# Optimization experiments

Hardware: AMD Instinct MI355X
Metric: run time of the kernel (lower is better)

## Reference

```python
import jax, jax.numpy as jnp
import numpy as np

N = 20000   # genes
E = 160000  # directed edges (self-loops added in forward, as PyG GATv2Conv does by default)
D = 64      # input feature dim
H1, C1 = 8, 128  # conv1 heads / channels
LRELU_SLOPE = 0.2
LN_EPS = 1e-5


def setup_inputs() -> dict:
    key = jax.random.key(0)
    ks = jax.random.split(key, 20)
    s = 0.05
    inp = {
        "x": jax.random.normal(ks[0], (N, D), dtype=jnp.float32),
        "edge_index": jax.random.randint(ks[1], (2, E), 0, N, dtype=jnp.int64),
        # conv1 (GATv2Conv D -> H1*C1, concat)
        "Wl1": jax.random.normal(ks[2], (D, H1 * C1), dtype=jnp.float32) * s,
        "bl1": jax.random.normal(ks[3], (H1 * C1,), dtype=jnp.float32) * s,
        "Wr1": jax.random.normal(ks[4], (D, H1 * C1), dtype=jnp.float32) * s,
        "br1": jax.random.normal(ks[5], (H1 * C1,), dtype=jnp.float32) * s,
        "att1": jax.random.normal(ks[6], (H1, C1), dtype=jnp.float32) * s,
        "b1": jax.random.normal(ks[7], (H1 * C1,), dtype=jnp.float32) * s,
        # skip Linear(D -> H1*C1)
        "Wskip": jax.random.normal(ks[8], (D, H1 * C1), dtype=jnp.float32) * s,
        "bskip": jax.random.normal(ks[9], (H1 * C1,), dtype=jnp.float32) * s,
        # LayerNorm(H1*C1)
        "g1": jnp.ones((H1 * C1,), dtype=jnp.float32),
        "beta1": jnp.zeros((H1 * C1,), dtype=jnp.float32),
        # conv2 (GATv2Conv H1*C1 -> 2, heads=1, concat=False)
        "Wl2": jax.random.normal(ks[10], (H1 * C1, 2), dtype=jnp.float32) * s,
        "bl2": jax.random.normal(ks[11], (2,), dtype=jnp.float32) * s,
        "Wr2": jax.random.normal(ks[12], (H1 * C1, 2), dtype=jnp.float32) * s,
        "br2": jax.random.normal(ks[13], (2,), dtype=jnp.float32) * s,
        "att2": jax.random.normal(ks[14], (1, 2), dtype=jnp.float32) * s,
        "b2": jax.random.normal(ks[15], (2,), dtype=jnp.float32) * s,
    }
    return inp


def _gatv2(x, src, dst, Wl, bl, Wr, br, att, bias, heads, ch, concat):
    """PyG GATv2Conv (eval mode): message src -> dst, scatter-softmax over dst."""
    n = x.shape[0]
    xl = (x @ Wl + bl).reshape(n, heads, ch)  # source-side transform
    xr = (x @ Wr + br).reshape(n, heads, ch)  # target-side transform
    e = jax.nn.leaky_relu(xl[src] + xr[dst], LRELU_SLOPE)   # [E,H,C]
    alpha = jnp.einsum('ehc,hc->eh', e, att)                 # [E,H]
    amax = jax.ops.segment_max(alpha, dst, num_segments=n)   # [N,H]
    ex = jnp.exp(alpha - amax[dst])
    denom = jax.ops.segment_sum(ex, dst, num_segments=n)
    alpha = ex / (denom[dst] + 1e-16)
    msg = xl[src] * alpha[..., None]                          # [E,H,C]
    out = jax.ops.segment_sum(msg, dst, num_segments=n)      # [N,H,C]
    out = out.reshape(n, heads * ch) if concat else out.mean(axis=1)
    return out + bias


def _layernorm(x, g, b):
    mu = x.mean(axis=-1, keepdims=True)
    var = ((x - mu) ** 2).mean(axis=-1, keepdims=True)
    return (x - mu) * jax.lax.rsqrt(var + LN_EPS) * g + b


def reference(x, edge_index, Wl1, bl1, Wr1, br1, att1, b1, Wskip, bskip,
              g1, beta1, Wl2, bl2, Wr2, br2, att2, b2):
    n = x.shape[0]
    loop = jnp.arange(n, dtype=edge_index.dtype)  # add_self_loops=True (PyG default)
    src = jnp.concatenate([edge_index[0], loop])
    dst = jnp.concatenate([edge_index[1], loop])
    x1 = _gatv2(x, src, dst, Wl1, bl1, Wr1, br1, att1, b1, H1, C1, True) + (x @ Wskip + bskip)
    x1 = jax.nn.elu(_layernorm(x1, g1, beta1))
    # dropout is a no-op in eval mode
    return _gatv2(x1, src, dst, Wl2, bl2, Wr2, br2, att2, b2, 1, 2, False)
```

## Files before the change

### kernel.cpp

```cpp
#include <hip/hip_runtime.h>
#include <hip/hip_bf16.h>
#include <hip/hip_fp16.h>
#include <math.h>

static constexpr int D  = 64;
static constexpr int F1 = 1024;
static constexpr int NTOT = 3072;

typedef _Float16 f16x8 __attribute__((ext_vector_type(8)));
typedef _Float16 h2    __attribute__((ext_vector_type(2)));
typedef float    f32x4 __attribute__((ext_vector_type(4)));
typedef unsigned int u32x4 __attribute__((ext_vector_type(4)));

__device__ __forceinline__ float lrelu(float x) { return x > 0.f ? x : 0.2f * x; }

__device__ __forceinline__ float dot2f(h2 a, h2 b, float c) {
#if __has_builtin(__builtin_amdgcn_fdot2)
    return __builtin_amdgcn_fdot2(a, b, c, false);
#else
    return c + (float)a[0] * (float)b[0] + (float)a[1] * (float)b[1];
#endif
}

__device__ __forceinline__ float red16(float p) {
    int v = __builtin_bit_cast(int, p);
    p += __builtin_bit_cast(float, __builtin_amdgcn_mov_dpp(v, 0xB1, 0xF, 0xF, true));
    v = __builtin_bit_cast(int, p);
    p += __builtin_bit_cast(float, __builtin_amdgcn_mov_dpp(v, 0x4E, 0xF, 0xF, true));
    v = __builtin_bit_cast(int, p);
    p += __builtin_bit_cast(float, __builtin_amdgcn_mov_dpp(v, 0x141, 0xF, 0xF, true));
    v = __builtin_bit_cast(int, p);
    p += __builtin_bit_cast(float, __builtin_amdgcn_mov_dpp(v, 0x140, 0xF, 0xF, true));
    return p;
}

union U4H { uint4 u; h2 h[4]; };

__global__ __launch_bounds__(256) void k_prep(
    const float* __restrict__ x, _Float16* __restrict__ xh,
    const int* __restrict__ ei, int* __restrict__ deg,
    const float* __restrict__ Wl1, const float* __restrict__ Wr1,
    const float* __restrict__ Wsk, _Float16* __restrict__ WhT,
    int n, int ne, int m, int castB, int degB)
{
    __shared__ _Float16 wt[128 * 72];
    const int b = blockIdx.x;
    if (b < castB) {
        int t = b * 256 + threadIdx.x;
        int ncast = (n * D) / 4;
        if (t < ncast) {
            float4 v = ((const float4*)x)[t];
            union { _Float16 h[4]; uint2 u; } o;
            o.h[0] = (_Float16)v.x; o.h[1] = (_Float16)v.y;
            o.h[2] = (_Float16)v.z; o.h[3] = (_Float16)v.w;
            *(uint2*)(xh + (size_t)t * 4) = o.u;
        }
    } else if (b < castB + degB) {
        int t = (b - castB) * 256 + threadIdx.x;
        if (t < m) {
            int d = (t < ne) ? ei[ne + t] : t - ne;
            atomicAdd(&deg[d], 1);
        }
    } else {
        const int t = threadIdx.x;
        const int c0 = (b - castB - degB) * 128;
        const float* __restrict__ W = (c0 < 1024) ? Wl1 : (c0 < 2048) ? Wr1 : Wsk;
        const int cw = c0 & 1023;
#pragma unroll
        for (int q = 0; q < 8; ++q) {
            int idx = t + 256 * q;
            int k = idx >> 5, c4 = (idx & 31) * 4;
            float4 v = *(const float4*)(W + (size_t)k * F1 + cw + c4);
            wt[(c4 + 0) * 72 + k] = (_Float16)v.x;
            wt[(c4 + 1) * 72 + k] = (_Float16)v.y;
            wt[(c4 + 2) * 72 + k] = (_Float16)v.z;
            wt[(c4 + 3) * 72 + k] = (_Float16)v.w;
        }
        __syncthreads();
#pragma unroll
        for (int q = 0; q < 4; ++q) {
            int idx = t + 256 * q;
            int c = idx >> 3, k0 = (idx & 7) * 8;
            uint4 v = *(const uint4*)(&wt[c * 72 + k0]);
            *(uint4*)(WhT + (size_t)(c0 + c) * 64 + k0) = v;
        }
    }
}

__global__ __launch_bounds__(1024) void k_scan(const int* __restrict__ deg,
                                               int* __restrict__ rowptr, int n)
{
    __shared__ int sums[1024];
    const int t = threadIdx.x;
    const int chunk = (n + 1023) / 1024;
    const int base = t * chunk;
    int s = 0;
    for (int i = 0; i < chunk; ++i) {
        int idx = base + i;
        if (idx < n) s += deg[idx];
    }
    sums[t] = s;
    __syncthreads();
    for (int off = 1; off < 1024; off <<= 1) {
        int v = (t >= off) ? sums[t - off] : 0;
        __syncthreads();
        sums[t] += v;
        __syncthreads();
    }
    int run = (t == 0) ? 0 : sums[t - 1];
    for (int i = 0; i < chunk; ++i) {
        int idx = base + i;
        if (idx < n) { rowptr[idx] = run; run += deg[idx]; }
    }
    if (t == 0) rowptr[n] = sums[1023];
}

#define AS(r, c) smem[(r) * 72 + (c)]
#define BS(r, c) smem[128 * 72 + (r) * 72 + (c)]
#define CS(r, c) smem[(r) * 136 + (c)]
__global__ __launch_bounds__(256) void k_gemm_mfma(
    const _Float16* __restrict__ xh, const _Float16* __restrict__ WhT,
    const float* __restrict__ bl1, const float* __restrict__ br1,
    const float* __restrict__ bsk, const float* __restrict__ b1,
    _Float16* __restrict__ xl1h, _Float16* __restrict__ xr1h,
    _Float16* __restrict__ sk1h,
    const int* __restrict__ ei, const int* __restrict__ rowptr,
    int* __restrict__ cursor, int* __restrict__ csr_off,
    int n, int ne, int m)
{
    extern __shared__ _Float16 smem[];
    const int t  = threadIdx.x;

    if (blockIdx.y == gridDim.y - 1) {
        const int stride = gridDim.x * 256;
        for (int e = blockIdx.x * 256 + t; e < m; e += stride) {
            int s, d;
            if (e < ne) { s = ei[e]; d = ei[ne + e]; }
            else        { s = e - ne; d = s; }
            int pos = rowptr[d] + atomicAdd(&cursor[d], 1);
            csr_off[pos] = s << 11;
        }
        return;
    }

    const int r0 = blockIdx.x * 128;
    const int c0 = blockIdx.y * 128;

#pragma unroll
    for (int q = 0; q < 4; ++q) {
        int c = t + 256 * q;
        int row = c >> 3, off = (c & 7) * 8;
        uint4 v = make_uint4(0, 0, 0, 0);
        if (r0 + row < n) v = *(const uint4*)(xh + (size_t)(r0 + row) * 64 + off);
        *(uint4*)(&AS(row, off)) = v;
        uint4 w = *(const uint4*)(WhT + (size_t)(c0 + row) * 64 + off);
        *(uint4*)(&BS(row, off)) = w;
    }
    __syncthreads();

    const int wave = t >> 6, lane = t & 63;
    const int quad = lane >> 4, l16 = lane & 15;
    const int mw = (wave & 1) * 64, nw = (wave >> 1) * 64;

    f16x8 bfrag[4][2];
#pragma unroll
    for (int nt = 0; nt < 4; ++nt)
#pragma unroll
        for (int ks = 0; ks < 2; ++ks)
            bfrag[nt][ks] = *(const f16x8*)(&BS(nw + nt * 16 + l16, ks * 32 + quad * 8));

    f32x4 acc[4][4];
#pragma unroll
    for (int mt = 0; mt < 4; ++mt)
#pragma unroll
        for (int nt = 0; nt < 4; ++nt) acc[mt][nt] = (f32x4){0.f, 0.f, 0.f, 0.f};

#pragma unroll
    for (int mt = 0; mt < 4; ++mt) {
        f16x8 af[2];
#pragma unroll
        for (int ks = 0; ks < 2; ++ks)
            af[ks] = *(const f16x8*)(&AS(mw + mt * 16 + l16, ks * 32 + quad * 8));
#pragma unroll
        for (int nt = 0; nt < 4; ++nt)
#pragma unroll
            for (int ks = 0; ks < 2; ++ks)
                acc[mt][nt] = __builtin_amdgcn_mfma_f32_16x16x32_f16(
                    af[ks], bfrag[nt][ks], acc[mt][nt], 0, 0, 0);
    }

    const int which = c0 >> 10;
    const int csec  = c0 & 1023;
    __syncthreads();
#pragma unroll
    for (int nt = 0; nt < 4; ++nt) {
        int col = csec + nw + nt * 16 + l16;
        float bias = (which == 0) ? bl1[col] : (which == 1) ? br1[col]
                                             : (bsk[col] + b1[col]);
#pragma unroll
        for (int mt = 0; mt < 4; ++mt) {
#pragma unroll
            for (int r = 0; r < 4; ++r)
                CS(mw + mt * 16 + quad * 4 + r, nw + nt * 16 + l16) =
                    (_Float16)(acc[mt][nt][r] + bias);
        }
    }
    __syncthreads();

    _Float16* __restrict__ dst = (which == 0) ? xl1h : (which == 1) ? xr1h : sk1h;
#pragma unroll
    for (int it = 0; it < 8; ++it) {
        int idx = t + 256 * it;
        int row = idx >> 4, c16 = idx & 15;
        int grow = r0 + row;
        if (grow < n) {
            u32x4 v = *(u32x4*)(&CS(row, c16 * 8));
            __builtin_nontemporal_store(v,
                (u32x4*)(dst + (size_t)grow * F1 + csec + c16 * 8));
        }
    }
}

__global__ __launch_bounds__(256, 4) void k_conv1_ln(
    const int* __restrict__ rowptr, const int* __restrict__ csr_off,
    const _Float16* __restrict__ xl1h, const _Float16* __restrict__ xr1h,
    const _Float16* __restrict__ sk1h,
    const float* __restrict__ att1,
    const float* __restrict__ g1, const float* __restrict__ beta1,
    const float* __restrict__ Wl2, const float* __restrict__ bl2,
    const float* __restrict__ Wr2, const float* __restrict__ br2,
    float* __restrict__ xl2, float* __restrict__ xr2, int n)
{
    __shared__ float sb[2][2][6];
    const int slot = threadIdx.x >> 7;
    const int q    = (threadIdx.x >> 6) & 1;
    const int lane = threadIdx.x & 63;
    const int node = blockIdx.x * 2 + slot;
    const bool active = node < n;
    const int cb  = q * 512 + lane * 8;
    const int cbB = cb * 2;
    const h2 c02 = (h2){(_Float16)0.2f, (_Float16)0.2f};
    const char* __restrict__ xlB = (const char*)xl1h;

    h2 xrv[4], at2[4], O[4];
    float ll = 0.f;
    float v[8];
    float s1 = 0.f, s2 = 0.f;

    if (active) {
        U4H u; u.u = *(const uint4*)(xr1h + (size_t)node * F1 + cb);
#pragma unroll
        for (int j = 0; j < 4; ++j) xrv[j] = u.h[j];
        float4 a0 = *(const float4*)(att1 + cb);
        float4 a1 = *(const float4*)(att1 + cb + 4);
        at2[0] = (h2){(_Float16)a0.x, (_Float16)a0.y};
        at2[1] = (h2){(_Float16)a0.z, (_Float16)a0.w};
        at2[2] = (h2){(_Float16)a1.x, (_Float16)a1.y};
        at2[3] = (h2){(_Float16)a1.z, (_Float16)a1.w};
#pragma unroll
        for (int j = 0; j < 4; ++j) O[j] = (h2){(_Float16)0.f, (_Float16)0.f};

        const int beg = rowptr[node], end = rowptr[node + 1];
        const int deg = end - beg;

        auto edge = [&](const U4H& cur) {
            float p = 0.f;
#pragma unroll
            for (int j = 0; j < 4; ++j) {
                h2 s = cur.h[j] + xrv[j];
                h2 r = __builtin_elementwise_max(s, s * c02);
                p = dot2f(r, at2[j], p);
            }
            p = red16(p);
            float w = __expf(p);
            ll += w;
            _Float16 wh = (_Float16)w;
            h2 wh2 = (h2){wh, wh};
#pragma unroll
            for (int j = 0; j < 4; ++j) O[j] = O[j] + wh2 * cur.h[j];
        };

        if (deg <= 64) {
            int offv = csr_off[beg + (lane < deg ? lane : 0)];
            auto ld = [&](int k) -> U4H {
                int kk = k < deg ? k : deg - 1;
                int off = __builtin_amdgcn_readlane(offv, kk);
                U4H u2; u2.u = *(const uint4*)(xlB + (unsigned)off + cbB);
                return u2;
            };
            U4H A0 = ld(0), A1 = ld(1), A2 = ld(2), A3 = ld(3);
            int i = 0;
            while (true) {
                bool more = (i + 4 < deg);
                U4H B0, B1, B2, B3;
                if (more) { B0 = ld(i + 4); B1 = ld(i + 5);
                            B2 = ld(i + 6); B3 = ld(i + 7); }
                edge(A0);
                if (i + 1 < deg) edge(A1);
                if (i + 2 < deg) edge(A2);
                if (i + 3 < deg) edge(A3);
                i += 4;
                if (!more) break;

                bool more2 = (i + 4 < deg);
                if (more2) { A0 = ld(i + 4); A1 = ld(i + 5);
                             A2 = ld(i + 6); A3 = ld(i + 7); }
                edge(B0);
                if (i + 1 < deg) edge(B1);
                if (i + 2 < deg) edge(B2);
                if (i + 3 < deg) edge(B3);
                i += 4;
                if (!more2) break;
            }
        } else {
            for (int e = beg; e < end; ++e) {
                U4H c;
                c.u = *(const uint4*)(xlB + (size_t)(unsigned)csr_off[e] + cbB);
                edge(c);
            }
        }

        float inv = 1.f / (ll + 1e-16f);
        U4H su; su.u = *(const uint4*)(sk1h + (size_t)node * F1 + cb);
#pragma unroll
        for (int j = 0; j < 4; ++j) {
            float xv0 = (float)su.h[j][0] + (float)O[j][0] * inv;
            float xv1 = (float)su.h[j][1] + (float)O[j][1] * inv;
            v[2 * j]     = xv0;
            v[2 * j + 1] = xv1;
            s1 += xv0 + xv1;
            s2 += xv0 * xv0 + xv1 * xv1;
        }
    }
#pragma unroll
    for (int off = 32; off > 0; off >>= 1) {
        s1 += __shfl_xor(s1, off);
        s2 += __shfl_xor(s2, off);
    }
    if (lane == 0) { sb[slot][q][0] = s1; sb[slot][q][1] = s2; }
    __syncthreads();
    float mu  = (sb[slot][0][0] + sb[slot][1][0]) * (1.f / 1024.f);
    float ms  = (sb[slot][0][1] + sb[slot][1][1]) * (1.f / 1024.f);
    float var = fmaxf(ms - mu * mu, 0.f);
    float inv = rsqrtf(var + 1e-5f);

    float p0 = 0.f, p1 = 0.f, p2 = 0.f, p3 = 0.f;
    if (active) {
        float4 gA = *(const float4*)(g1 + cb),    gB = *(const float4*)(g1 + cb + 4);
        float4 bA = *(const float4*)(beta1 + cb), bB = *(const float4*)(beta1 + cb + 4);
        float gv[8] = {gA.x, gA.y, gA.z, gA.w, gB.x, gB.y, gB.z, gB.w};
        float bv[8] = {bA.x, bA.y, bA.z, bA.w, bB.x, bB.y, bB.z, bB.w};
#pragma unroll
        for (int j = 0; j < 8; j += 2) {
            float4 wl = *(const float4*)(Wl2 + (cb + j) * 2);
            float4 wr = *(const float4*)(Wr2 + (cb + j) * 2);
            float y0 = (v[j]   - mu) * inv * gv[j]   + bv[j];
            float y1 = (v[j+1] - mu) * inv * gv[j+1] + bv[j+1];
            float z0 = y0 > 0.f ? y0 : __expf(y0) - 1.f;
            float z1 = y1 > 0.f ? y1 : __expf(y1) - 1.f;
            p0 += z0 * wl.x + z1 * wl.z;
            p1 += z0 * wl.y + z1 * wl.w;
            p2 += z0 * wr.x + z1 * wr.z;
            p3 += z0 * wr.y + z1 * wr.w;
        }
    }
#pragma unroll
    for (int off = 32; off > 0; off >>= 1) {
        p0 += __shfl_xor(p0, off); p1 += __shfl_xor(p1, off);
        p2 += __shfl_xor(p2, off); p3 += __shfl_xor(p3, off);
    }
    if (lane == 0) { sb[slot][q][2] = p0; sb[slot][q][3] = p1;
                     sb[slot][q][4] = p2; sb[slot][q][5] = p3; }
    __syncthreads();
    if (active && lane == 0 && q == 0) {
        xl2[node * 2 + 0] = sb[slot][0][2] + sb[slot][1][2] + bl2[0];
        xl2[node * 2 + 1] = sb[slot][0][3] + sb[slot][1][3] + bl2[1];
        xr2[node * 2 + 0] = sb[slot][0][4] + sb[slot][1][4] + br2[0];
        xr2[node * 2 + 1] = sb[slot][0][5] + sb[slot][1][5] + br2[1];
    }
}

__global__ __launch_bounds__(64) void k_conv2(
    const int* __restrict__ rowptr, const int* __restrict__ csr_off,
    const float* __restrict__ xl2, const float* __restrict__ xr2,
    const float* __restrict__ att2, const float* __restrict__ b2,
    float* __restrict__ out2, int n)
{
    int d = blockIdx.x * blockDim.x + threadIdx.x;
    if (d >= n) return;
    float2 xr = *(const float2*)(xr2 + 2 * d);
    float a0w = att2[0], a1w = att2[1];
    float m = -INFINITY, l = 0.f, o0 = 0.f, o1 = 0.f;
    const int beg = rowptr[d], end = rowptr[d + 1];
    float2 pf[2];
    pf[0] = *(const float2*)(xl2 + (csr_off[beg] >> 10));
    pf[1] = (beg + 1 < end) ? *(const float2*)(xl2 + (csr_off[beg + 1] >> 10)) : pf[0];
    for (int i = beg; i < end; ++i) {
        float2 cur = pf[0];
        pf[0] = pf[1];
        if (i + 2 < end) pf[1] = *(const float2*)(xl2 + (csr_off[i + 2] >> 10));
        float p = lrelu(cur.x + xr.x) * a0w + lrelu(cur.y + xr.y) * a1w;
        float nm = fmaxf(m, p);
        float sc = __expf(m - nm);
        float w  = __expf(p - nm);
        l = l * sc + w;
        o0 = o0 * sc + w * cur.x;
        o1 = o1 * sc + w * cur.y;
        m = nm;
    }
    float inv = 1.f / (l + 1e-16f);
    out2[2 * d + 0] = o0 * inv + b2[0];
    out2[2 * d + 1] = o1 * inv + b2[1];
}

extern "C" void kernel_launch(void* const* d_in, const int* in_sizes, int n_in,
                              void* d_out, int out_size, void* d_ws, size_t ws_size,
                              hipStream_t stream)
{
    const float* x     = (const float*)d_in[0];
    const int*   ei    = (const int*)  d_in[1];
    const float* Wl1   = (const float*)d_in[2];
    const float* bl1   = (const float*)d_in[3];
    const float* Wr1   = (const float*)d_in[4];
    const float* br1   = (const float*)d_in[5];
    const float* att1  = (const float*)d_in[6];
    const float* b1    = (const float*)d_in[7];
    const float* Wsk   = (const float*)d_in[8];
    const float* bsk   = (const float*)d_in[9];
    const float* g1    = (const float*)d_in[10];
    const float* beta1 = (const float*)d_in[11];
    const float* Wl2   = (const float*)d_in[12];
    const float* bl2   = (const float*)d_in[13];
    const float* Wr2   = (const float*)d_in[14];
    const float* br2   = (const float*)d_in[15];
    const float* att2  = (const float*)d_in[16];
    const float* b2    = (const float*)d_in[17];

    const int n  = in_sizes[0] / D;
    const int ne = in_sizes[1] / 2;
    const int m  = ne + n;

    float* ws = (float*)d_ws;
    size_t o = 0;
    _Float16* xl1h = (_Float16*)(ws + o); o += (size_t)n * F1 / 2;
    _Float16* xr1h = (_Float16*)(ws + o); o += (size_t)n * F1 / 2;
    _Float16* sk1h = (_Float16*)(ws + o); o += (size_t)n * F1 / 2;
    _Float16* xh   = (_Float16*)(ws + o); o += (size_t)n * D / 2;
    _Float16* WhT  = (_Float16*)(ws + o); o += (size_t)NTOT * 64 / 2;
    float* xl2    = ws + o; o += (size_t)n * 2;
    float* xr2    = ws + o; o += (size_t)n * 2;
    int* rowptr   = (int*)(ws + o); o += (size_t)n + 1;
    int* deg      = (int*)(ws + o); o += (size_t)n;
    int* cursor   = (int*)(ws + o); o += (size_t)n;
    int* csr_off  = (int*)(ws + o); o += (size_t)m;
    float* out2   = (float*)d_out;

    (void)hipMemsetAsync(deg, 0, (size_t)2 * n * sizeof(int), stream);
    const int castB = ((n * D) / 4 + 255) / 256;
    const int degB  = (m + 255) / 256;
    k_prep<<<castB + degB + NTOT / 128, 256, 0, stream>>>(
        x, xh, ei, deg, Wl1, Wr1, Wsk, WhT, n, ne, m, castB, degB);
    k_scan<<<1, 1024, 0, stream>>>(deg, rowptr, n);

    dim3 gg((n + 127) / 128, NTOT / 128 + 1);
    k_gemm_mfma<<<gg, 256, 36864, stream>>>(xh, WhT, bl1, br1, bsk, b1,
                                            xl1h, xr1h, sk1h,
                                            ei, rowptr, cursor, csr_off,
                                            n, ne, m);

    k_conv1_ln<<<(n + 1) / 2, 256, 0, stream>>>(rowptr, csr_off, xl1h, xr1h, sk1h,
                                                att1, g1, beta1, Wl2, bl2, Wr2, br2,
                                                xl2, xr2, n);

    k_conv2<<<(n + 63) / 64, 64, 0, stream>>>(rowptr, csr_off, xl2, xr2, att2, b2, out2, n);
}
```

Baseline: 241.6 us.

## Map one wavefront per node in conv1 aggregation, dropping cross-wave LDS reduction

```diff
diff --git a/kernel.cpp b/kernel.cpp
--- a/kernel.cpp
+++ b/kernel.cpp
@@ -22,19 +22,17 @@
 #endif
 }
 
-__device__ __forceinline__ float red16(float p) {
+__device__ __forceinline__ float red8(float p) {
     int v = __builtin_bit_cast(int, p);
     p += __builtin_bit_cast(float, __builtin_amdgcn_mov_dpp(v, 0xB1, 0xF, 0xF, true));
     v = __builtin_bit_cast(int, p);
     p += __builtin_bit_cast(float, __builtin_amdgcn_mov_dpp(v, 0x4E, 0xF, 0xF, true));
     v = __builtin_bit_cast(int, p);
     p += __builtin_bit_cast(float, __builtin_amdgcn_mov_dpp(v, 0x141, 0xF, 0xF, true));
-    v = __builtin_bit_cast(int, p);
-    p += __builtin_bit_cast(float, __builtin_amdgcn_mov_dpp(v, 0x140, 0xF, 0xF, true));
     return p;
 }
 
-union U4H { uint4 u; h2 h[4]; };
+union U8H { uint4 u[2]; h2 h[8]; };
 
 __global__ __launch_bounds__(256) void k_prep(
     const float* __restrict__ x, _Float16* __restrict__ xh,
@@ -215,8 +213,7 @@
         int grow = r0 + row;
         if (grow < n) {
             u32x4 v = *(u32x4*)(&CS(row, c16 * 8));
-            __builtin_nontemporal_store(v,
-                (u32x4*)(dst + (size_t)grow * F1 + csec + c16 * 8));
+            *(u32x4*)(dst + (size_t)grow * F1 + csec + c16 * 8) = v;
         }
     }
 }
@@ -231,99 +228,101 @@
     const float* __restrict__ Wr2, const float* __restrict__ br2,
     float* __restrict__ xl2, float* __restrict__ xr2, int n)
 {
-    __shared__ float sb[2][2][6];
-    const int slot = threadIdx.x >> 7;
-    const int q    = (threadIdx.x >> 6) & 1;
     const int lane = threadIdx.x & 63;
-    const int node = blockIdx.x * 2 + slot;
-    const bool active = node < n;
-    const int cb  = q * 512 + lane * 8;
-    const int cbB = cb * 2;
+    const int wid  = threadIdx.x >> 6;
+    const int node = blockIdx.x * 4 + wid;
+    if (node >= n) return;
+
+    const int cb  = lane * 16;
+    const int cbB = lane * 32;
     const h2 c02 = (h2){(_Float16)0.2f, (_Float16)0.2f};
     const char* __restrict__ xlB = (const char*)xl1h;
 
-    h2 xrv[4], at2[4], O[4];
+    h2 xrv[8], at2[8], O[8];
+    {
+        U8H u;
+        u.u[0] = *(const uint4*)(xr1h + (size_t)node * F1 + cb);
+        u.u[1] = *(const uint4*)(xr1h + (size_t)node * F1 + cb + 8);
+#pragma unroll
+        for (int j = 0; j < 8; ++j) xrv[j] = u.h[j];
+    }
+#pragma unroll
+    for (int j = 0; j < 4; ++j) {
+        float4 a = *(const float4*)(att1 + cb + 4 * j);
+        at2[2 * j]     = (h2){(_Float16)a.x, (_Float16)a.y};
+        at2[2 * j + 1] = (h2){(_Float16)a.z, (_Float16)a.w};
+    }
+#pragma unroll
+    for (int j = 0; j < 8; ++j) O[j] = (h2){(_Float16)0.f, (_Float16)0.f};
+
     float ll = 0.f;
-    float v[8];
+    const int beg = rowptr[node], end = rowptr[node + 1];
+    const int deg = end - beg;
+
+    auto edge = [&](const U8H& cur) {
+        float p = 0.f;
+#pragma unroll
+        for (int j = 0; j < 8; ++j) {
+            h2 s = cur.h[j] + xrv[j];
+            h2 r = __builtin_elementwise_max(s, s * c02);
+            p = dot2f(r, at2[j], p);
+        }
+        p = red8(p);
+        float w = __expf(p);
+        ll += w;
+        _Float16 wh = (_Float16)w;
+        h2 wh2 = (h2){wh, wh};
+#pragma unroll
+        for (int j = 0; j < 8; ++j) O[j] = O[j] + wh2 * cur.h[j];
+    };
+
+    if (deg <= 64) {
+        int offv = csr_off[beg + (lane < deg ? lane : 0)];
+        auto ld = [&](int k) -> U8H {
+            int kk = k < deg ? k : deg - 1;
+            int off = __builtin_amdgcn_readlane(offv, kk);
+            U8H u2;
+            u2.u[0] = *(const uint4*)(xlB + (unsigned)off + cbB);
+            u2.u[1] = *(const uint4*)(xlB + (unsigned)off + cbB + 16);
+            return u2;
+        };
+        U8H A0 = ld(0), A1 = ld(1);
+        int i = 0;
+        while (true) {
+            bool more = (i + 2 < deg);
+            U8H B0, B1;
+            if (more) { B0 = ld(i + 2); B1 = ld(i + 3); }
+            edge(A0);
+            if (i + 1 < deg) edge(A1);
+            i += 2;
+            if (!more) break;
+
+            bool more2 = (i + 2 < deg);
+            if (more2) { A0 = ld(i + 2); A1 = ld(i + 3); }
+            edge(B0);
+            if (i + 1 < deg) edge(B1);
+            i += 2;
+            if (!more2) break;
+        }
+    } else {
+        for (int e = beg; e < end; ++e) {
+            U8H c;
+            const char* p = xlB + (size_t)(unsigned)csr_off[e] + cbB;
+            c.u[0] = *(const uint4*)(p);
+            c.u[1] = *(const uint4*)(p + 16);
+            edge(c);
+        }
+    }
+
+    float v[16];
     float s1 = 0.f, s2 = 0.f;
-
-    if (active) {
-        U4H u; u.u = *(const uint4*)(xr1h + (size_t)node * F1 + cb);
-#pragma unroll
-        for (int j = 0; j < 4; ++j) xrv[j] = u.h[j];
-        float4 a0 = *(const float4*)(att1 + cb);
-        float4 a1 = *(const float4*)(att1 + cb + 4);
-        at2[0] = (h2){(_Float16)a0.x, (_Float16)a0.y};
-        at2[1] = (h2){(_Float16)a0.z, (_Float16)a0.w};
-        at2[2] = (h2){(_Float16)a1.x, (_Float16)a1.y};
-        at2[3] = (h2){(_Float16)a1.z, (_Float16)a1.w};
-#pragma unroll
-        for (int j = 0; j < 4; ++j) O[j] = (h2){(_Float16)0.f, (_Float16)0.f};
-
-        const int beg = rowptr[node], end = rowptr[node + 1];
-        const int deg = end - beg;
-
-        auto edge = [&](const U4H& cur) {
-            float p = 0.f;
-#pragma unroll
-            for (int j = 0; j < 4; ++j) {
-                h2 s = cur.h[j] + xrv[j];
-                h2 r = __builtin_elementwise_max(s, s * c02);
-                p = dot2f(r, at2[j], p);
-            }
-            p = red16(p);
-            float w = __expf(p);
-            ll += w;
-            _Float16 wh = (_Float16)w;
-            h2 wh2 = (h2){wh, wh};
-#pragma unroll
-            for (int j = 0; j < 4; ++j) O[j] = O[j] + wh2 * cur.h[j];
-        };
-
-        if (deg <= 64) {
-            int offv = csr_off[beg + (lane < deg ? lane : 0)];
-            auto ld = [&](int k) -> U4H {
-                int kk = k < deg ? k : deg - 1;
-                int off = __builtin_amdgcn_readlane(offv, kk);
-                U4H u2; u2.u = *(const uint4*)(xlB + (unsigned)off + cbB);
-                return u2;
-            };
-            U4H A0 = ld(0), A1 = ld(1), A2 = ld(2), A3 = ld(3);
-            int i = 0;
-            while (true) {
-                bool more = (i + 4 < deg);
-                U4H B0, B1, B2, B3;
-                if (more) { B0 = ld(i + 4); B1 = ld(i + 5);
-                            B2 = ld(i + 6); B3 = ld(i + 7); }
-                edge(A0);
-                if (i + 1 < deg) edge(A1);
-                if (i + 2 < deg) edge(A2);
-                if (i + 3 < deg) edge(A3);
-                i += 4;
-                if (!more) break;
-
-                bool more2 = (i + 4 < deg);
-                if (more2) { A0 = ld(i + 4); A1 = ld(i + 5);
-                             A2 = ld(i + 6); A3 = ld(i + 7); }
-                edge(B0);
-                if (i + 1 < deg) edge(B1);
-                if (i + 2 < deg) edge(B2);
-                if (i + 3 < deg) edge(B3);
-                i += 4;
-                if (!more2) break;
-            }
-        } else {
-            for (int e = beg; e < end; ++e) {
-                U4H c;
-                c.u = *(const uint4*)(xlB + (size_t)(unsigned)csr_off[e] + cbB);
-                edge(c);
-            }
-        }
-
+    {
         float inv = 1.f / (ll + 1e-16f);
-        U4H su; su.u = *(const uint4*)(sk1h + (size_t)node * F1 + cb);
-#pragma unroll
-        for (int j = 0; j < 4; ++j) {
+        U8H su;
+        su.u[0] = *(const uint4*)(sk1h + (size_t)node * F1 + cb);
+        su.u[1] = *(const uint4*)(sk1h + (size_t)node * F1 + cb + 8);
+#pragma unroll
+        for (int j = 0; j < 8; ++j) {
             float xv0 = (float)su.h[j][0] + (float)O[j][0] * inv;
             float xv1 = (float)su.h[j][1] + (float)O[j][1] * inv;
             v[2 * j]     = xv0;
@@ -337,21 +336,23 @@
         s1 += __shfl_xor(s1, off);
         s2 += __shfl_xor(s2, off);
     }
-    if (lane == 0) { sb[slot][q][0] = s1; sb[slot][q][1] = s2; }
-    __syncthreads();
-    float mu  = (sb[slot][0][0] + sb[slot][1][0]) * (1.f / 1024.f);
-    float ms  = (sb[slot][0][1] + sb[slot][1][1]) * (1.f / 1024.f);
+    float mu  = s1 * (1.f / 1024.f);
+    float ms  = s2 * (1.f / 1024.f);
     float var = fmaxf(ms - mu * mu, 0.f);
     float inv = rsqrtf(var + 1e-5f);
 
     float p0 = 0.f, p1 = 0.f, p2 = 0.f, p3 = 0.f;
-    if (active) {
-        float4 gA = *(const float4*)(g1 + cb),    gB = *(const float4*)(g1 + cb + 4);
-        float4 bA = *(const float4*)(beta1 + cb), bB = *(const float4*)(beta1 + cb + 4);
-        float gv[8] = {gA.x, gA.y, gA.z, gA.w, gB.x, gB.y, gB.z, gB.w};
-        float bv[8] = {bA.x, bA.y, bA.z, bA.w, bB.x, bB.y, bB.z, bB.w};
-#pragma unroll
-        for (int j = 0; j < 8; j += 2) {
+    {
+        float gv[16], bv[16];
+#pragma unroll
+        for (int j = 0; j < 4; ++j) {
+            float4 g = *(const float4*)(g1 + cb + 4 * j);
+            float4 b = *(const float4*)(beta1 + cb + 4 * j);
+            gv[4*j] = g.x; gv[4*j+1] = g.y; gv[4*j+2] = g.z; gv[4*j+3] = g.w;
+            bv[4*j] = b.x; bv[4*j+1] = b.y; bv[4*j+2] = b.z; bv[4*j+3] = b.w;
+        }
+#pragma unroll
+        for (int j = 0; j < 16; j += 2) {
             float4 wl = *(const float4*)(Wl2 + (cb + j) * 2);
             float4 wr = *(const float4*)(Wr2 + (cb + j) * 2);
             float y0 = (v[j]   - mu) * inv * gv[j]   + bv[j];
@@ -369,14 +370,11 @@
         p0 += __shfl_xor(p0, off); p1 += __shfl_xor(p1, off);
         p2 += __shfl_xor(p2, off); p3 += __shfl_xor(p3, off);
     }
-    if (lane == 0) { sb[slot][q][2] = p0; sb[slot][q][3] = p1;
-                     sb[slot][q][4] = p2; sb[slot][q][5] = p3; }
-    __syncthreads();
-    if (active && lane == 0 && q == 0) {
-        xl2[node * 2 + 0] = sb[slot][0][2] + sb[slot][1][2] + bl2[0];
-        xl2[node * 2 + 1] = sb[slot][0][3] + sb[slot][1][3] + bl2[1];
-        xr2[node * 2 + 0] = sb[slot][0][4] + sb[slot][1][4] + br2[0];
-        xr2[node * 2 + 1] = sb[slot][0][5] + sb[slot][1][5] + br2[1];
+    if (lane == 0) {
+        float2 ol = make_float2(p0 + bl2[0], p1 + bl2[1]);
+        float2 orr = make_float2(p2 + br2[0], p3 + br2[1]);
+        *(float2*)(xl2 + 2 * node) = ol;
+        *(float2*)(xr2 + 2 * node) = orr;
     }
 }
 
@@ -468,7 +466,7 @@
                                             ei, rowptr, cursor, csr_off,
                                             n, ne, m);
 
-    k_conv1_ln<<<(n + 1) / 2, 256, 0, stream>>>(rowptr, csr_off, xl1h, xr1h, sk1h,
+    k_conv1_ln<<<(n + 3) / 4, 256, 0, stream>>>(rowptr, csr_off, xl1h, xr1h, sk1h,
                                                 att1, g1, beta1, Wl2, bl2, Wr2, br2,
                                                 xl2, xr2, n);
 
```

After: 267.5 us. +10.7%, slower.
